# Kernel tuning notes

Hardware: AMD Instinct MI355X
Metric: run time of the kernel (lower is better)

The kernel has to match this reference:

```python
import jax, jax.numpy as jnp
import numpy as np
from jax import lax

D = 256      # d_model
NH = 4       # nhead == len(multi_size)
DH = D // NH # per-head dim = 64
B, H, W = 8, 32, 32
EPS_LN = 1e-5
EPS_ATT = 1e-6


def conv2d(x, w, pad):
    # x: [B,C,H,W], w: [O,I,k,k], SAME padding via pad=k//2
    return lax.conv_general_dilated(
        x, w, window_strides=(1, 1), padding=[(pad, pad), (pad, pad)],
        dimension_numbers=("NCHW", "OIHW", "NCHW"))


def layer_norm(x, g, b):
    m = jnp.mean(x, axis=-1, keepdims=True)
    v = jnp.mean((x - m) ** 2, axis=-1, keepdims=True)
    return (x - m) * lax.rsqrt(v + EPS_LN) * g + b


def setup_inputs() -> dict:
    key = jax.random.key(0)
    ks = jax.random.split(key, 20)
    s = 0.02
    inp = {
        "x": jax.random.normal(ks[0], (B, D, H, W), jnp.float32),
        "source": jax.random.normal(ks[1], (B, D, H, W), jnp.float32),
        # q projection: conv3x3 d_model -> d_model (bias-free)
        "Wq": jax.random.normal(ks[2], (D, D, 3, 3), jnp.float32) * s,
        # MultiConv k projection: kernels 1,3,5,7, each d_model -> dim
        "Wk1": jax.random.normal(ks[3], (DH, D, 1, 1), jnp.float32) * s,
        "Wk3": jax.random.normal(ks[4], (DH, D, 3, 3), jnp.float32) * s,
        "Wk5": jax.random.normal(ks[5], (DH, D, 5, 5), jnp.float32) * s,
        "Wk7": jax.random.normal(ks[6], (DH, D, 7, 7), jnp.float32) * s,
        # MultiConv v projection
        "Wv1": jax.random.normal(ks[7], (DH, D, 1, 1), jnp.float32) * s,
        "Wv3": jax.random.normal(ks[8], (DH, D, 3, 3), jnp.float32) * s,
        "Wv5": jax.random.normal(ks[9], (DH, D, 5, 5), jnp.float32) * s,
        "Wv7": jax.random.normal(ks[10], (DH, D, 7, 7), jnp.float32) * s,
        # merge linear (bias=False), stored [in,out]
        "Wm": jax.random.normal(ks[11], (D, D), jnp.float32) * s,
        "ln1_g": jnp.ones((D,), jnp.float32),
        "ln1_b": jnp.zeros((D,), jnp.float32),
        "ln2_g": jnp.ones((D,), jnp.float32),
        "ln2_b": jnp.zeros((D,), jnp.float32),
        # FF mlp: Linear(2D->2D, no bias), ReLU, Linear(2D->D, no bias); [in,out]
        "W1": jax.random.normal(ks[12], (2 * D, 2 * D), jnp.float32) * s,
        "W2": jax.random.normal(ks[13], (2 * D, D), jnp.float32) * s,
    }
    return inp


def _forward(x, source, Wq, Wk1, Wk3, Wk5, Wk7, Wv1, Wv3, Wv5, Wv7,
             Wm, ln1_g, ln1_b, ln2_g, ln2_b, W1, W2):
    b, c, h, w = x.shape
    h1, w1 = source.shape[2], source.shape[3]
    L = h * w
    S = h1 * w1

    # projections (multi-scale convs -> heads along channel)
    q = conv2d(x, Wq, 1)                                        # [b,D,h,w]
    k = jnp.concatenate([conv2d(source, Wk1, 0), conv2d(source, Wk3, 1),
                         conv2d(source, Wk5, 2), conv2d(source, Wk7, 3)], axis=1)
    v = jnp.concatenate([conv2d(source, Wv1, 0), conv2d(source, Wv3, 1),
                         conv2d(source, Wv5, 2), conv2d(source, Wv7, 3)], axis=1)

    # b c h w -> b (h w) (nhead dim) -> b L nhead dim
    q = q.transpose(0, 2, 3, 1).reshape(b, L, NH, DH)
    k = k.transpose(0, 2, 3, 1).reshape(b, S, NH, DH)
    v = v.transpose(0, 2, 3, 1).reshape(b, S, NH, DH)

    # FullAttention_vis: softmax attention map [b, L, S, nhead]
    temp = DH ** -0.5
    qk = jnp.einsum("blhd,bshd->blsh", q, k)
    attn_vis = jax.nn.softmax(qk * temp, axis=2)

    # LinearAttention (elu+1 kernel feature map)
    Qf = jax.nn.elu(q) + 1.0
    Kf = jax.nn.elu(k) + 1.0
    v_len = jnp.float32(S)
    vals = v / v_len
    KV = jnp.einsum("bshd,bshv->bhdv", Kf, vals)                # [b,NH,DH,DH]
    Z = 1.0 / (jnp.einsum("blhd,bhd->blh", Qf, Kf.sum(axis=1)) + EPS_ATT)
    msg = jnp.einsum("blhd,bhdv,blh->blhv", Qf, KV, Z) * v_len  # [b,L,NH,DH]

    # merge + norm1
    msg = layer_norm(msg.reshape(b, L, D) @ Wm, ln1_g, ln1_b)

    # FF (mlp): cat -> Linear -> ReLU -> Linear -> norm2
    xf = x.transpose(0, 2, 3, 1).reshape(b, L, c)
    ff = jax.nn.relu(jnp.concatenate([xf, msg], axis=2) @ W1) @ W2
    msg = layer_norm(ff, ln2_g, ln2_b)                          # [b,L,D]
    msg = msg.reshape(b, h, w, c).transpose(0, 3, 1, 2)         # b c h w

    out = x + msg
    # b (h0 w0) (h1 w1) c -> b c h0 w0 h1 w1
    vis = attn_vis.reshape(b, h, w, h1, w1, NH).transpose(0, 5, 1, 2, 3, 4)
    return out, vis


def reference(x, source, Wq, Wk1, Wk3, Wk5, Wk7, Wv1, Wv3, Wv5, Wv7,
              Wm, ln1_g, ln1_b, ln2_g, ln2_b, W1, W2):
    return _forward(x, source, Wq, Wk1, Wk3, Wk5, Wk7, Wv1, Wv3, Wv5, Wv7,
                    Wm, ln1_g, ln1_b, ln2_g, ln2_b, W1, W2)
```

## Files before the change

### kernel.cpp

```cpp
#include <hip/hip_runtime.h>

#define DEV __device__ __forceinline__

typedef unsigned short u16;
typedef unsigned int u32;
typedef __bf16 bf16x8 __attribute__((ext_vector_type(8)));
typedef float f32x4 __attribute__((ext_vector_type(4)));

DEV float elu1(float x) { return x > 0.f ? x + 1.f : __expf(x); }

DEV u16 f2bf(float f) {
    union { float f; unsigned u; } v; v.f = f;
    unsigned r = v.u + 0x7fffu + ((v.u >> 16) & 1u);
    return (u16)(r >> 16);
}

DEV float bf2f(u16 h) {
    union { u32 u; float f; } v; v.u = ((u32)h) << 16; return v.f;
}

__global__ __launch_bounds__(256) void prep1_kernel(
    const float* __restrict__ Wq,
    const float* __restrict__ Wk1, const float* __restrict__ Wk3,
    const float* __restrict__ Wk5, const float* __restrict__ Wk7,
    const float* __restrict__ Wv1, const float* __restrict__ Wv3,
    const float* __restrict__ Wv5, const float* __restrict__ Wv7,
    u16* __restrict__ wpack,
    const float* __restrict__ x, const float* __restrict__ src,
    u16* __restrict__ xbh, u16* __restrict__ sbh)
{
    __shared__ float lds[32 * 129];
    const int t = threadIdx.x;
    if (blockIdx.x < 1632) {
        int gid = blockIdx.x * 256 + t;
        int frag = gid >> 6, l = gid & 63;
        const float* W; int K, ocbase = 0, rel;
        if (frag < 1152) {
            W = Wq; K = 3; int slot = frag / 288; rel = frag % 288; ocbase = slot * 64;
        } else {
            int f = frag - 1152; int side = f / 2688; f %= 2688;
            if (f < 32)        { W = side ? Wv1 : Wk1; K = 1; rel = f; }
            else if (f < 320)  { W = side ? Wv3 : Wk3; K = 3; rel = f - 32; }
            else if (f < 1120) { W = side ? Wv5 : Wk5; K = 5; rel = f - 320; }
            else               { W = side ? Wv7 : Wk7; K = 7; rel = f - 1120; }
        }
        int og = rel & 3, cc = (rel >> 2) & 7, tap = rel >> 5;
        int dy = tap / K, dx = tap % K;
        int oc = ocbase + og * 16 + (l & 15);
        int c0 = cc * 32 + (l >> 4) * 8;
        u16 pk[8];
#pragma unroll
        for (int j = 0; j < 8; ++j)
            pk[j] = f2bf(W[((size_t)(oc * 256 + c0 + j) * K + dy) * K + dx]);
        *(int4*)&wpack[(size_t)frag * 512 + l * 8] = *(const int4*)pk;
        return;
    }
    const int i = blockIdx.x - 1632;
    const int inp = i >> 9, rem = i & 511;
    const int b = rem >> 6, cc = (rem >> 3) & 7, pxb = rem & 7;
    const float* in = (inp ? src : x) + ((size_t)b * 256 + cc * 32) * 1024 + pxb * 128;
    u16* outp = (inp ? sbh : xbh) + (size_t)b * 262144 + (size_t)cc * 32768 + pxb * 128 * 32;
#pragma unroll
    for (int u = 0; u < 4; ++u) {
        int unit = t + u * 256;
        int r = unit >> 5, px4 = unit & 31;
        float4 v = *(const float4*)(in + (size_t)r * 1024 + px4 * 4);
        lds[r * 129 + px4 * 4 + 0] = v.x;
        lds[r * 129 + px4 * 4 + 1] = v.y;
        lds[r * 129 + px4 * 4 + 2] = v.z;
        lds[r * 129 + px4 * 4 + 3] = v.w;
    }
    __syncthreads();
#pragma unroll
    for (int u = 0; u < 2; ++u) {
        int unit = t + u * 256;
        int px = unit >> 2, cg = unit & 3;
        u16 pk[8];
#pragma unroll
        for (int j = 0; j < 8; ++j) pk[j] = f2bf(lds[(cg * 8 + j) * 129 + px]);
        *(int4*)&outp[px * 32 + cg * 8] = *(const int4*)pk;
    }
}

template<int K>
DEV void conv_mfma_body(const u16* __restrict__ srcb,
                        const u16* __restrict__ wsec,
                        float* __restrict__ dst,
                        u16* Bt, int y0, int cch0, int ncc, int t)
{
    constexpr int P = K / 2;
    const int w = t >> 6, l = t & 63;
    const int chi = l >> 4, ln = l & 15;
    const int rowbase = chi * 22 + w * 2 + 3 - P;
    const int colbase = ln + 3 - P;
    f32x4 acc[4][4];
#pragma unroll
    for (int m = 0; m < 4; ++m)
#pragma unroll
        for (int n = 0; n < 4; ++n) acc[m][n] = (f32x4){0.f, 0.f, 0.f, 0.f};

    for (int cc = 0; cc < ncc; ++cc) {
        const int ccg = cch0 + cc;
        __syncthreads();
#pragma unroll
        for (int u = 0; u < 7; ++u) {
            int unit = t + (u << 9);
            if (unit < 2816) {
                int xv = unit & 31, r = unit >> 5;
                int yy = r % 22, ch = r / 22;
                int ygl = y0 - 3 + yy;
                int4 pk;
                if ((unsigned)ygl < 32u)
                    pk = *(const int4*)&srcb[(size_t)ccg * 32768 + (ygl * 32 + xv) * 32 + ch * 8];
                else
                    pk = (int4){0, 0, 0, 0};
                *(int4*)&Bt[((ch * 22 + yy) * 40 + xv + 3) * 8] = pk;
            } else if (unit < 3520) {
                int hu = unit - 2816;
                int hx = hu & 7; int xi = hx < 3 ? hx : hx + 32;
                int r = hu >> 3; int yy = r % 22, ch = r / 22;
                int4 z = {0, 0, 0, 0};
                *(int4*)&Bt[((ch * 22 + yy) * 40 + xi) * 8] = z;
            }
        }
        __syncthreads();
#pragma unroll
        for (int dy = 0; dy < K; ++dy) {
#pragma unroll
            for (int dx = 0; dx < K; ++dx) {
                const int tap = dy * K + dx;
                const u16* wp = wsec + ((size_t)(tap * 8 + ccg) * 4) * 512 + l * 8;
                bf16x8 a0 = *(const bf16x8*)(wp);
                bf16x8 a1 = *(const bf16x8*)(wp + 512);
                bf16x8 a2 = *(const bf16x8*)(wp + 1024);
                bf16x8 a3 = *(const bf16x8*)(wp + 1536);
                bf16x8 bf[4];
#pragma unroll
                for (int n = 0; n < 4; ++n) {
                    int row = rowbase + dy + (n >> 1);
                    int col = colbase + dx + (n & 1) * 16;
                    bf[n] = *(const bf16x8*)&Bt[(row * 40 + col) * 8];
                }
#pragma unroll
                for (int n = 0; n < 4; ++n) {
                    acc[0][n] = __builtin_amdgcn_mfma_f32_16x16x32_bf16(a0, bf[n], acc[0][n], 0, 0, 0);
                    acc[1][n] = __builtin_amdgcn_mfma_f32_16x16x32_bf16(a1, bf[n], acc[1][n], 0, 0, 0);
                    acc[2][n] = __builtin_amdgcn_mfma_f32_16x16x32_bf16(a2, bf[n], acc[2][n], 0, 0, 0);
                    acc[3][n] = __builtin_amdgcn_mfma_f32_16x16x32_bf16(a3, bf[n], acc[3][n], 0, 0, 0);
                }
            }
        }
    }
#pragma unroll
    for (int m = 0; m < 4; ++m)
#pragma unroll
        for (int n = 0; n < 4; ++n) {
            int y = y0 + w * 2 + (n >> 1);
            int px = y * 32 + (n & 1) * 16 + ln;
            int ocb = m * 16 + chi * 4;
#pragma unroll
            for (int r = 0; r < 4; ++r)
                dst[(size_t)(ocb + r) * 1024 + px] = acc[m][n][r];
        }
}

__global__ __launch_bounds__(512) void conv_mfma_kernel(
    const u16* __restrict__ xbh, const u16* __restrict__ sbh,
    const u16* __restrict__ wpack,
    float* __restrict__ qb, float* __restrict__ kb, float* __restrict__ vb,
    float* __restrict__ p5, float* __restrict__ p7)
{
    __shared__ u16 Bt[4 * 22 * 40 * 8];
    const int bx = blockIdx.x, t = threadIdx.x;
    const int g = bx & 31, b = (bx >> 5) & 7, m = bx >> 8;
    if (g < 4) {
        conv_mfma_body<3>(xbh + (size_t)b * 262144,
                          wpack + (size_t)(g * 288) * 512,
                          qb + ((size_t)b * 256 + g * 64) * 1024,
                          Bt, m * 16, 0, 8, t);
        return;
    }
    const int gs = g - 4;
    const int side = gs / 14, gg = gs % 14;
    const u16* sp = sbh + (size_t)b * 262144;
    float* fin = side ? vb : kb;
    const size_t wkb = 1152 + (size_t)side * 2688;
    if (gg == 0) {
        conv_mfma_body<1>(sp, wpack + (wkb + 0) * 512,
                          fin + ((size_t)b * 256) * 1024, Bt, m * 16, 0, 8, t);
    } else if (gg == 1) {
        conv_mfma_body<3>(sp, wpack + (wkb + 32) * 512,
                          fin + ((size_t)b * 256 + 64) * 1024, Bt, m * 16, 0, 8, t);
    } else if (gg < 6) {
        int cpart = gg - 2;
        conv_mfma_body<5>(sp, wpack + (wkb + 320) * 512,
                          p5 + (((size_t)side * 4 + cpart) * 8 + b) * 65536,
                          Bt, m * 16, cpart * 2, 2, t);
    } else {
        int cpart = gg - 6;
        conv_mfma_body<7>(sp, wpack + (wkb + 1120) * 512,
                          p7 + (((size_t)side * 8 + cpart) * 8 + b) * 65536,
                          Bt, m * 16, cpart, 1, t);
    }
}

__global__ __launch_bounds__(256) void prep2_kernel(
    const float* __restrict__ p5, const float* __restrict__ p7,
    float* __restrict__ kb, float* __restrict__ vb,
    const float* __restrict__ W1, const float* __restrict__ W2,
    const float* __restrict__ Wm,
    u16* __restrict__ w1p, u16* __restrict__ w2p, u16* __restrict__ wmp)
{
    const int t = threadIdx.x;
    if (blockIdx.x < 2048) {
        int gid = blockIdx.x * 256 + t;
        int px4 = gid & 255;
        int rr = gid >> 8;
        int oc = rr & 63, b = (rr >> 6) & 7, head = (rr >> 9) & 1, side = rr >> 10;
        float* outb = side ? vb : kb;
        float4 s = make_float4(0.f, 0.f, 0.f, 0.f);
        if (head == 0) {
#pragma unroll
            for (int p = 0; p < 4; ++p) {
                float4 u = *((const float4*)(p5 + (((size_t)side * 4 + p) * 8 + b) * 65536 + (size_t)oc * 1024) + px4);
                s.x += u.x; s.y += u.y; s.z += u.z; s.w += u.w;
            }
            *((float4*)(outb + ((size_t)b * 256 + 128 + oc) * 1024) + px4) = s;
        } else {
#pragma unroll
            for (int p = 0; p < 8; ++p) {
                float4 u = *((const float4*)(p7 + (((size_t)side * 8 + p) * 8 + b) * 65536 + (size_t)oc * 1024) + px4);
                s.x += u.x; s.y += u.y; s.z += u.z; s.w += u.w;
            }
            *((float4*)(outb + ((size_t)b * 256 + 192 + oc) * 1024) + px4) = s;
        }
        return;
    }
    int gid = (blockIdx.x - 2048) * 256 + t;
    int f = gid >> 6, l = gid & 63;
    if (f >= 896) return;
    u16 pk[8];
    if (f < 512) {
        int ks = f >> 5, nf = f & 31;
#pragma unroll
        for (int j = 0; j < 8; ++j)
            pk[j] = f2bf(W1[(size_t)(ks * 32 + (l >> 4) * 8 + j) * 512 + nf * 16 + (l & 15)]);
        *(int4*)&w1p[(size_t)f * 512 + l * 8] = *(const int4*)pk;
    } else if (f < 768) {
        int f2 = f - 512;
        int ks = f2 >> 4, nf = f2 & 15;
#pragma unroll
        for (int j = 0; j < 8; ++j)
            pk[j] = f2bf(W2[(size_t)(ks * 32 + (l >> 4) * 8 + j) * 256 + nf * 16 + (l & 15)]);
        *(int4*)&w2p[(size_t)f2 * 512 + l * 8] = *(const int4*)pk;
    } else {
        int f3 = f - 768;
        int ks = f3 >> 4, nf = f3 & 15;
#pragma unroll
        for (int j = 0; j < 8; ++j)
            pk[j] = f2bf(Wm[(size_t)(ks * 32 + (l >> 4) * 8 + j) * 256 + nf * 16 + (l & 15)]);
        *(int4*)&wmp[(size_t)f3 * 512 + l * 8] = *(const int4*)pk;
    }
}

__global__ __launch_bounds__(256) void prep3_kernel(
    const float* __restrict__ qb, const float* __restrict__ kb,
    const float* __restrict__ vb,
    u16* __restrict__ qbt, u16* __restrict__ kbt,
    float* __restrict__ KVp, float* __restrict__ Ksump)
{
    __shared__ float4 smem4[2112];
    const int t = threadIdx.x;
    if (blockIdx.x < 1024) {
        float* lds = (float*)smem4;
        const int i = blockIdx.x;
        const int inp = i >> 9, rem = i & 511;
        const int b = rem >> 6, h = (rem >> 4) & 3, pxb = rem & 15;
        const float* in = (inp ? kb : qb) + ((size_t)b * 256 + h * 64) * 1024 + pxb * 64;
        u16* outp = (inp ? kbt : qbt) + (((size_t)(b * 4 + h)) * 1024 + pxb * 64) * 64;
#pragma unroll
        for (int u = 0; u < 4; ++u) {
            int unit = t + u * 256;
            int r = unit >> 4, px4 = unit & 15;
            float4 v = *(const float4*)(in + (size_t)r * 1024 + px4 * 4);
            lds[r * 65 + px4 * 4 + 0] = v.x;
            lds[r * 65 + px4 * 4 + 1] = v.y;
            lds[r * 65 + px4 * 4 + 2] = v.z;
            lds[r * 65 + px4 * 4 + 3] = v.w;
        }
        __syncthreads();
#pragma unroll
        for (int u = 0; u < 2; ++u) {
            int unit = t + u * 256;
            int px = unit >> 3, cg = unit & 7;
            u16 pk[8];
#pragma unroll
            for (int j = 0; j < 8; ++j) pk[j] = f2bf(lds[(cg * 8 + j) * 65 + px]);
            *(int4*)&outp[px * 64 + cg * 8] = *(const int4*)pk;
        }
        return;
    }
    float4* Kt4 = smem4;
    float4* Vt4 = smem4 + 64 * 17;
    float* Kt = (float*)Kt4;
    float* Vt = (float*)Vt4;
    const int bx = blockIdx.x - 1024;
    const int b = bx >> 4, h = (bx >> 2) & 3, ch = bx & 3;
    const float* kp = kb + ((size_t)b * 256 + h * 64) * 1024 + ch * 256;
    const float* vp = vb + ((size_t)b * 256 + h * 64) * 1024 + ch * 256;
    const int d = t >> 2, v0 = (t & 3) * 16;
    float4 acc[4];
#pragma unroll
    for (int j = 0; j < 4; ++j) acc[j] = make_float4(0.f, 0.f, 0.f, 0.f);
    float ks = 0.f;
    for (int st = 0; st < 4; ++st) {
        __syncthreads();
        {
            int dd = t >> 2, r0 = (t & 3) * 16;
#pragma unroll
            for (int mm = 0; mm < 4; ++mm) {
                float4 kv = *(const float4*)(kp + dd * 1024 + st * 64 + r0 + mm * 4);
                Kt[(r0 + mm * 4 + 0) * 68 + dd] = elu1(kv.x);
                Kt[(r0 + mm * 4 + 1) * 68 + dd] = elu1(kv.y);
                Kt[(r0 + mm * 4 + 2) * 68 + dd] = elu1(kv.z);
                Kt[(r0 + mm * 4 + 3) * 68 + dd] = elu1(kv.w);
                float4 vv = *(const float4*)(vp + dd * 1024 + st * 64 + r0 + mm * 4);
                Vt[(r0 + mm * 4 + 0) * 64 + dd] = vv.x;
                Vt[(r0 + mm * 4 + 1) * 64 + dd] = vv.y;
                Vt[(r0 + mm * 4 + 2) * 64 + dd] = vv.z;
                Vt[(r0 + mm * 4 + 3) * 64 + dd] = vv.w;
            }
        }
        __syncthreads();
#pragma unroll 8
        for (int s = 0; s < 64; ++s) {
            float kf = Kt[s * 68 + d];
            const float4* vvp = (const float4*)(Vt + s * 64 + v0);
#pragma unroll
            for (int j = 0; j < 4; ++j) {
                float4 vv = vvp[j];
                acc[j].x += kf * vv.x; acc[j].y += kf * vv.y;
                acc[j].z += kf * vv.z; acc[j].w += kf * vv.w;
            }
        }
        if (t < 64) {
#pragma unroll 8
            for (int s = 0; s < 64; ++s) ks += Kt[s * 68 + t];
        }
    }
    float* op = KVp + ((size_t)((ch * 32 + b * 4 + h) * 64 + d)) * 64 + v0;
#pragma unroll
    for (int j = 0; j < 4; ++j) ((float4*)op)[j] = acc[j];
    if (t < 64) Ksump[(size_t)(ch * 32 + b * 4 + h) * 64 + t] = ks;
}

__global__ __launch_bounds__(512) void qk_sm_msg_kernel(
    const u16* __restrict__ qbt, const u16* __restrict__ kbt,
    float* __restrict__ vis,
    const float* __restrict__ KVp, const float* __restrict__ Ksump,
    float* __restrict__ msg)
{
    __shared__ float4 smem4[4178];
    const int t = threadIdx.x;
    if (blockIdx.x < 1024) {
        u16* kf = (u16*)smem4;
        u16* qf = (u16*)smem4 + 32 * 512;
        float* redM = (float*)((char*)smem4 + 36864);
        float* redS = redM + 256;
        const int bx = blockIdx.x;
        const int b = bx >> 7, h = (bx >> 5) & 3, l0 = (bx & 31) * 32;
        const u16* qtp = qbt + ((size_t)(b * 4 + h)) * 1024 * 64;
        const u16* ktp = kbt + ((size_t)(b * 4 + h)) * 1024 * 64;

        if (t < 256) {
            int r = t & 31, dblk = t >> 5;
            int4 pk = *(const int4*)&qtp[(size_t)(l0 + r) * 64 + dblk * 8];
            *(int4*)&qf[(((r >> 4) * 2 + (dblk >> 2)) * 64 + (dblk & 3) * 16 + (r & 15)) * 8] = pk;
        }
        __syncthreads();

        const int w = t >> 6, l = t & 63, ln = l & 15, lg = l >> 4;
        bf16x8 a[2][2];
#pragma unroll
        for (int fr = 0; fr < 2; ++fr)
#pragma unroll
            for (int ks = 0; ks < 2; ++ks)
                a[fr][ks] = *(const bf16x8*)&qf[((fr * 2 + ks) * 64 + l) * 8];

        f32x4 acc[2][4][2];
#pragma unroll
        for (int fr = 0; fr < 2; ++fr)
#pragma unroll
            for (int cc = 0; cc < 4; ++cc)
#pragma unroll
                for (int f = 0; f < 2; ++f) acc[fr][cc][f] = (f32x4){0.f, 0.f, 0.f, 0.f};

#pragma unroll
        for (int cc = 0; cc < 4; ++cc) {
            __syncthreads();
#pragma unroll
            for (int it = 0; it < 4; ++it) {
                int unit = it * 512 + t;
                int sl = unit & 255, dblk = unit >> 8;
                int4 pk = *(const int4*)&ktp[(size_t)(cc * 256 + sl) * 64 + dblk * 8];
                *(int4*)&kf[(((sl >> 4) * 2 + (dblk >> 2)) * 64 + (dblk & 3) * 16 + (sl & 15)) * 8] = pk;
            }
            __syncthreads();
#pragma unroll
            for (int f = 0; f < 2; ++f) {
                int fg = (w * 2 + f) * 2;
                bf16x8 b0 = *(const bf16x8*)&kf[((fg + 0) * 64 + l) * 8];
                bf16x8 b1 = *(const bf16x8*)&kf[((fg + 1) * 64 + l) * 8];
#pragma unroll
                for (int fr = 0; fr < 2; ++fr) {
                    acc[fr][cc][f] = __builtin_amdgcn_mfma_f32_16x16x32_bf16(a[fr][0], b0, acc[fr][cc][f], 0, 0, 0);
                    acc[fr][cc][f] = __builtin_amdgcn_mfma_f32_16x16x32_bf16(a[fr][1], b1, acc[fr][cc][f], 0, 0, 0);
                }
            }
        }

#pragma unroll
        for (int fr = 0; fr < 2; ++fr)
#pragma unroll
            for (int cc = 0; cc < 4; ++cc)
#pragma unroll
                for (int f = 0; f < 2; ++f)
#pragma unroll
                    for (int e = 0; e < 4; ++e) acc[fr][cc][f][e] *= 0.125f;

        float rmax[2][4];
#pragma unroll
        for (int fr = 0; fr < 2; ++fr)
#pragma unroll
            for (int reg = 0; reg < 4; ++reg) {
                float m = -1e30f;
#pragma unroll
                for (int cc = 0; cc < 4; ++cc)
#pragma unroll
                    for (int f = 0; f < 2; ++f) m = fmaxf(m, acc[fr][cc][f][reg]);
#pragma unroll
                for (int off = 1; off < 16; off <<= 1) m = fmaxf(m, __shfl_xor(m, off));
                if (ln == 0) redM[(fr * 16 + lg * 4 + reg) * 8 + w] = m;
                rmax[fr][reg] = m;
            }
        __syncthreads();
#pragma unroll
        for (int fr = 0; fr < 2; ++fr)
#pragma unroll
            for (int reg = 0; reg < 4; ++reg) {
                int r = fr * 16 + lg * 4 + reg;
                float m = redM[r * 8];
#pragma unroll
                for (int ww = 1; ww < 8; ++ww) m = fmaxf(m, redM[r * 8 + ww]);
                rmax[fr][reg] = m;
            }
#pragma unroll
        for (int fr = 0; fr < 2; ++fr)
#pragma unroll
            for (int reg = 0; reg < 4; ++reg) {
                float s = 0.f;
                float m = rmax[fr][reg];
#pragma unroll
                for (int cc = 0; cc < 4; ++cc)
#pragma unroll
                    for (int f = 0; f < 2; ++f) {
                        float e = __expf(acc[fr][cc][f][reg] - m);
                        acc[fr][cc][f][reg] = e;
                        s += e;
                    }
#pragma unroll
                for (int off = 1; off < 16; off <<= 1) s += __shfl_xor(s, off);
                if (ln == 0) redS[(fr * 16 + lg * 4 + reg) * 8 + w] = s;
            }
        __syncthreads();
        float invv[2][4];
#pragma unroll
        for (int fr = 0; fr < 2; ++fr)
#pragma unroll
            for (int reg = 0; reg < 4; ++reg) {
                int r = fr * 16 + lg * 4 + reg;
                float s = redS[r * 8] + redS[r * 8 + 1] + redS[r * 8 + 2] + redS[r * 8 + 3]
                        + redS[r * 8 + 4] + redS[r * 8 + 5] + redS[r * 8 + 6] + redS[r * 8 + 7];
                invv[fr][reg] = 1.f / s;
            }
        float* outT = (float*)smem4;
        float* visp = vis + (((size_t)(b * 4 + h)) << 20);
#pragma unroll
        for (int cc = 0; cc < 4; ++cc) {
            __syncthreads();
#pragma unroll
            for (int fr = 0; fr < 2; ++fr)
#pragma unroll
                for (int reg = 0; reg < 4; ++reg) {
                    int r = fr * 16 + lg * 4 + reg;
#pragma unroll
                    for (int f = 0; f < 2; ++f)
                        outT[r * 260 + w * 32 + f * 16 + ln] = acc[fr][cc][f][reg] * invv[fr][reg];
                }
            __syncthreads();
#pragma unroll
            for (int u = 0; u < 4; ++u) {
                int unit = u * 512 + t;
                int r = unit >> 6, c4 = unit & 63;
                float4 v = *(const float4*)&outT[r * 260 + c4 * 4];
                *(float4*)&visp[(size_t)(l0 + r) * 1024 + cc * 256 + c4 * 4] = v;
            }
        }
        return;
    }
    float* kvl = (float*)smem4;
    float* ksl = (float*)smem4 + 4 * 4112;
    const int bx2 = blockIdx.x - 1024;
    const int b = bx2 >> 3, l0 = (bx2 & 7) * 128;
#pragma unroll
    for (int m = 0; m < 8; ++m) {
        int unit = t + (m << 9);
        int hh = unit >> 10, dd = (unit >> 4) & 63, v4 = unit & 15;
        float4 s = make_float4(0.f, 0.f, 0.f, 0.f);
#pragma unroll
        for (int ch = 0; ch < 4; ++ch) {
            float4 u = *(const float4*)&KVp[((size_t)(ch * 32 + b * 4)) * 4096 + (size_t)unit * 4];
            s.x += u.x; s.y += u.y; s.z += u.z; s.w += u.w;
        }
        *(float4*)&kvl[hh * 4112 + dd * 64 + v4 * 4] = s;
    }
    if (t < 256) {
        float s = 0.f;
#pragma unroll
        for (int ch = 0; ch < 4; ++ch)
            s += Ksump[(size_t)(ch * 32 + b * 4) * 64 + t];
        ksl[(t >> 6) * 65 + (t & 63)] = s;
    }
    __syncthreads();
    const int h = t & 3, l = l0 + (t >> 2);
    const u16* qrow = qbt + ((size_t)(b * 4 + h) * 1024 + l) * 64;
    float qf[64];
#pragma unroll
    for (int j8 = 0; j8 < 8; ++j8) {
        int4 pk = *(const int4*)&qrow[j8 * 8];
        const u16* pku = (const u16*)&pk;
#pragma unroll
        for (int e = 0; e < 8; ++e) qf[j8 * 8 + e] = elu1(bf2f(pku[e]));
    }
    float zd = 1e-6f;
#pragma unroll
    for (int dd = 0; dd < 64; ++dd) zd += qf[dd] * ksl[h * 65 + dd];
    const float Z = 1.f / zd;
    float* op = msg + ((size_t)(b * 1024 + l)) * 256 + h * 64;
    for (int c0 = 0; c0 < 64; c0 += 16) {
        float4 a[4];
#pragma unroll
        for (int j = 0; j < 4; ++j) a[j] = make_float4(0.f, 0.f, 0.f, 0.f);
#pragma unroll
        for (int dd = 0; dd < 64; ++dd) {
            float qv = qf[dd];
            const float4* kp = (const float4*)(kvl + h * 4112 + dd * 64 + c0);
#pragma unroll
            for (int j = 0; j < 4; ++j) {
                float4 kk = kp[j];
                a[j].x += qv * kk.x; a[j].y += qv * kk.y;
                a[j].z += qv * kk.z; a[j].w += qv * kk.w;
            }
        }
#pragma unroll
        for (int j = 0; j < 4; ++j) {
            a[j].x *= Z; a[j].y *= Z; a[j].z *= Z; a[j].w *= Z;
            ((float4*)(op + c0))[j] = a[j];
        }
    }
}

__global__ __launch_bounds__(256) void ff_fused_kernel(
    const float* __restrict__ x, const float* __restrict__ msg,
    const u16* __restrict__ wmp,
    const u16* __restrict__ w1p, const u16* __restrict__ w2p,
    const float* __restrict__ g1, const float* __restrict__ b1,
    const float* __restrict__ g2, const float* __restrict__ b2,
    float* __restrict__ out)
{
    __shared__ u16 tile[16 * 520];
    __shared__ u16 mtile[16 * 264];
    __shared__ float redS[16 * 4];
    __shared__ float redQ[16 * 4];
    float* tf = (float*)tile;
    const int t = threadIdx.x;
    const int base = blockIdx.x * 16;
    const int b = base >> 10, l0 = base & 1023;
    const int w = t >> 6, l = t & 63, ln = l & 15, lg = l >> 4;

    {
        int rr = t & 15, cg = t >> 4;
        for (int cci = 0; cci < 16; ++cci) {
            int c = cci * 16 + cg;
            tile[rr * 520 + c] = f2bf(x[((size_t)b * 256 + c) * 1024 + l0 + rr]);
        }
        int r = t >> 4, cb = (t & 15) * 16;
#pragma unroll
        for (int i = 0; i < 4; ++i) {
            float4 v = *(const float4*)&msg[((size_t)(base + r)) * 256 + cb + i * 4];
            u32 p0 = (u32)f2bf(v.x) | ((u32)f2bf(v.y) << 16);
            u32 p1 = (u32)f2bf(v.z) | ((u32)f2bf(v.w) << 16);
            *(u32*)&mtile[r * 264 + cb + i * 4] = p0;
            *(u32*)&mtile[r * 264 + cb + i * 4 + 2] = p1;
        }
    }
    __syncthreads();

    f32x4 accm[4];
#pragma unroll
    for (int fc = 0; fc < 4; ++fc) accm[fc] = (f32x4){0.f, 0.f, 0.f, 0.f};
    for (int ks = 0; ks < 8; ++ks) {
        bf16x8 a0 = *(const bf16x8*)&mtile[ln * 264 + ks * 32 + lg * 8];
#pragma unroll
        for (int fc = 0; fc < 4; ++fc) {
            bf16x8 bb = *(const bf16x8*)&wmp[((size_t)(ks * 16 + w * 4 + fc) * 64 + l) * 8];
            accm[fc] = __builtin_amdgcn_mfma_f32_16x16x32_bf16(a0, bb, accm[fc], 0, 0, 0);
        }
    }
#pragma unroll
    for (int reg = 0; reg < 4; ++reg) {
        float s = 0.f, qsum = 0.f;
#pragma unroll
        for (int fc = 0; fc < 4; ++fc) {
            float v = accm[fc][reg];
            s += v; qsum += v * v;
        }
#pragma unroll
        for (int off = 1; off < 16; off <<= 1) {
            s += __shfl_xor(s, off);
            qsum += __shfl_xor(qsum, off);
        }
        if (ln == 0) {
            int r = lg * 4 + reg;
            redS[r * 4 + w] = s;
            redQ[r * 4 + w] = qsum;
        }
    }
    __syncthreads();
#pragma unroll
    for (int fc = 0; fc < 4; ++fc) {
        int c = w * 64 + fc * 16 + ln;
        float gg = g1[c], bb = b1[c];
#pragma unroll
        for (int reg = 0; reg < 4; ++reg) {
            int r = lg * 4 + reg;
            float s = redS[r * 4] + redS[r * 4 + 1] + redS[r * 4 + 2] + redS[r * 4 + 3];
            float qs = redQ[r * 4] + redQ[r * 4 + 1] + redQ[r * 4 + 2] + redQ[r * 4 + 3];
            float mean = s * (1.f / 256.f);
            float rstd = rsqrtf(qs * (1.f / 256.f) - mean * mean + 1e-5f);
            tile[r * 520 + 256 + c] = f2bf((accm[fc][reg] - mean) * rstd * gg + bb);
        }
    }
    __syncthreads();

    f32x4 acc1[8];
#pragma unroll
    for (int fc = 0; fc < 8; ++fc) acc1[fc] = (f32x4){0.f, 0.f, 0.f, 0.f};
    for (int ks = 0; ks < 16; ++ks) {
        bf16x8 a0 = *(const bf16x8*)&tile[ln * 520 + ks * 32 + lg * 8];
#pragma unroll
        for (int fc = 0; fc < 8; ++fc) {
            bf16x8 bb = *(const bf16x8*)&w1p[((size_t)(ks * 32 + w * 8 + fc) * 64 + l) * 8];
            acc1[fc] = __builtin_amdgcn_mfma_f32_16x16x32_bf16(a0, bb, acc1[fc], 0, 0, 0);
        }
    }
    __syncthreads();
#pragma unroll
    for (int fc = 0; fc < 8; ++fc)
#pragma unroll
        for (int reg = 0; reg < 4; ++reg) {
            int r = lg * 4 + reg;
            int c = w * 128 + fc * 16 + ln;
            tile[r * 520 + c] = f2bf(fmaxf(acc1[fc][reg], 0.f));
        }
    __syncthreads();

    f32x4 acc2[4];
#pragma unroll
    for (int fc = 0; fc < 4; ++fc) acc2[fc] = (f32x4){0.f, 0.f, 0.f, 0.f};
    for (int ks = 0; ks < 16; ++ks) {
        bf16x8 a0 = *(const bf16x8*)&tile[ln * 520 + ks * 32 + lg * 8];
#pragma unroll
        for (int fc = 0; fc < 4; ++fc) {
            bf16x8 bb = *(const bf16x8*)&w2p[((size_t)(ks * 16 + w * 4 + fc) * 64 + l) * 8];
            acc2[fc] = __builtin_amdgcn_mfma_f32_16x16x32_bf16(a0, bb, acc2[fc], 0, 0, 0);
        }
    }
#pragma unroll
    for (int reg = 0; reg < 4; ++reg) {
        float s = 0.f, qsum = 0.f;
#pragma unroll
        for (int fc = 0; fc < 4; ++fc) {
            float v = acc2[fc][reg];
            s += v; qsum += v * v;
        }
#pragma unroll
        for (int off = 1; off < 16; off <<= 1) {
            s += __shfl_xor(s, off);
            qsum += __shfl_xor(qsum, off);
        }
        if (ln == 0) {
            int r = lg * 4 + reg;
            redS[r * 4 + w] = s;
            redQ[r * 4 + w] = qsum;
        }
    }
    __syncthreads();
    float mean[4], rstd[4];
#pragma unroll
    for (int reg = 0; reg < 4; ++reg) {
        int r = lg * 4 + reg;
        float s = redS[r * 4] + redS[r * 4 + 1] + redS[r * 4 + 2] + redS[r * 4 + 3];
        float qs = redQ[r * 4] + redQ[r * 4 + 1] + redQ[r * 4 + 2] + redQ[r * 4 + 3];
        float m = s * (1.f / 256.f);
        mean[reg] = m;
        rstd[reg] = rsqrtf(qs * (1.f / 256.f) - m * m + 1e-5f);
    }
    __syncthreads();
#pragma unroll
    for (int fc = 0; fc < 4; ++fc) {
        int c = w * 64 + fc * 16 + ln;
        float gg = g2[c], bb = b2[c];
#pragma unroll
        for (int reg = 0; reg < 4; ++reg) {
            int r = lg * 4 + reg;
            tf[r * 260 + c] = (acc2[fc][reg] - mean[reg]) * rstd[reg] * gg + bb;
        }
    }
    __syncthreads();
    {
        const float* xp = x + ((size_t)b * 256 + t) * 1024 + l0;
        float* op = out + ((size_t)b * 256 + t) * 1024 + l0;
#pragma unroll
        for (int i = 0; i < 4; ++i) {
            float4 xv = *(const float4*)(xp + i * 4);
            float4 o;
            o.x = xv.x + tf[(i * 4 + 0) * 260 + t];
            o.y = xv.y + tf[(i * 4 + 1) * 260 + t];
            o.z = xv.z + tf[(i * 4 + 2) * 260 + t];
            o.w = xv.w + tf[(i * 4 + 3) * 260 + t];
            *(float4*)(op + i * 4) = o;
        }
    }
}

extern "C" void kernel_launch(void* const* d_in, const int* in_sizes, int n_in,
                              void* d_out, int out_size, void* d_ws, size_t ws_size,
                              hipStream_t stream)
{
    const float* x    = (const float*)d_in[0];
    const float* src  = (const float*)d_in[1];
    const float* Wq   = (const float*)d_in[2];
    const float* Wk1  = (const float*)d_in[3];
    const float* Wk3  = (const float*)d_in[4];
    const float* Wk5  = (const float*)d_in[5];
    const float* Wk7  = (const float*)d_in[6];
    const float* Wv1  = (const float*)d_in[7];
    const float* Wv3  = (const float*)d_in[8];
    const float* Wv5  = (const float*)d_in[9];
    const float* Wv7  = (const float*)d_in[10];
    const float* Wm   = (const float*)d_in[11];
    const float* g1   = (const float*)d_in[12];
    const float* b1   = (const float*)d_in[13];
    const float* g2   = (const float*)d_in[14];
    const float* b2   = (const float*)d_in[15];
    const float* W1   = (const float*)d_in[16];
    const float* W2   = (const float*)d_in[17];

    float* out = (float*)d_out;
    float* vis = out + 2097152;

    float* p5 = vis;
    float* p7 = vis + 4194304;

    float* ws    = (float*)d_ws;
    float* qb    = ws;
    float* kb    = ws + 2097152;
    float* vb    = ws + 4194304;
    u16*   wpack = (u16*)(ws + 6291456);
    u16*   w1p   = (u16*)(ws + 6291456);
    u16*   w2p   = (u16*)(ws + 6422528);
    u16*   wmp   = (u16*)(ws + 6488064);
    u16*   qbt   = (u16*)(ws + 6520832);
    u16*   kbt   = (u16*)(ws + 7569408);
    u16*   xbh   = (u16*)(ws + 7962624);
    u16*   sbh   = (u16*)(ws + 9011200);
    float* msg   = ws + 10059776;
    float* KVp   = ws + 12156928;
    float* Ksump = ws + 12681216;

    prep1_kernel    <<<2656, 256, 0, stream>>>(Wq, Wk1, Wk3, Wk5, Wk7,
                                               Wv1, Wv3, Wv5, Wv7, wpack,
                                               x, src, xbh, sbh);
    conv_mfma_kernel<<<512,  512, 0, stream>>>(xbh, sbh, wpack, qb, kb, vb, p5, p7);
    prep2_kernel    <<<2272, 256, 0, stream>>>(p5, p7, kb, vb,
                                               W1, W2, Wm, w1p, w2p, wmp);
    prep3_kernel    <<<1152, 256, 0, stream>>>(qb, kb, vb, qbt, kbt, KVp, Ksump);
    qk_sm_msg_kernel<<<1088, 512, 0, stream>>>(qbt, kbt, vis, KVp, Ksump, msg);
    ff_fused_kernel <<<512,  256, 0, stream>>>(x, msg, wmp, w1p, w2p,
                                               g1, b1, g2, b2, out);
}
```

Before: 269.1 us.

## Emit conv outputs as pixel-major bf16 and drop the separate transpose pass

The conv MFMA kernel now packs its accumulators to bf16 and writes them in pixel-major [px][64] layout, so the Q/K/V projections and the 5x5/7x7 partial sums no longer go through fp32 channel-major buffers. The split-K reduction in prep2 reads bf16 partials, and the transpose/convert half of prep3 is removed, which cuts several hundred blocks and a large amount of memory traffic. The attention-map store to vis now uses nontemporal stores. In exchange, partial sums are rounded to bf16 before they are reduced, which adds some error, and K/V reach the KV computation already rounded.

```diff
diff --git a/kernel.cpp b/kernel.cpp
--- a/kernel.cpp
+++ b/kernel.cpp
@@ -85,7 +85,7 @@
 template<int K>
 DEV void conv_mfma_body(const u16* __restrict__ srcb,
                         const u16* __restrict__ wsec,
-                        float* __restrict__ dst,
+                        u16* __restrict__ dst,
                         u16* Bt, int y0, int cch0, int ncc, int t)
 {
     constexpr int P = K / 2;
@@ -158,17 +158,18 @@
             int y = y0 + w * 2 + (n >> 1);
             int px = y * 32 + (n & 1) * 16 + ln;
             int ocb = m * 16 + chi * 4;
-#pragma unroll
-            for (int r = 0; r < 4; ++r)
-                dst[(size_t)(ocb + r) * 1024 + px] = acc[m][n][r];
+            u16 pk[4];
+#pragma unroll
+            for (int r = 0; r < 4; ++r) pk[r] = f2bf(acc[m][n][r]);
+            *(uint2*)&dst[(size_t)px * 64 + ocb] = *(const uint2*)pk;
         }
 }
 
 __global__ __launch_bounds__(512) void conv_mfma_kernel(
     const u16* __restrict__ xbh, const u16* __restrict__ sbh,
     const u16* __restrict__ wpack,
-    float* __restrict__ qb, float* __restrict__ kb, float* __restrict__ vb,
-    float* __restrict__ p5, float* __restrict__ p7)
+    u16* __restrict__ qbt, u16* __restrict__ kbt, u16* __restrict__ vbt,
+    u16* __restrict__ p5u, u16* __restrict__ p7u)
 {
     __shared__ u16 Bt[4 * 22 * 40 * 8];
     const int bx = blockIdx.x, t = threadIdx.x;
@@ -176,67 +177,76 @@
     if (g < 4) {
         conv_mfma_body<3>(xbh + (size_t)b * 262144,
                           wpack + (size_t)(g * 288) * 512,
-                          qb + ((size_t)b * 256 + g * 64) * 1024,
+                          qbt + ((size_t)(b * 4 + g)) * 65536,
                           Bt, m * 16, 0, 8, t);
         return;
     }
     const int gs = g - 4;
     const int side = gs / 14, gg = gs % 14;
     const u16* sp = sbh + (size_t)b * 262144;
-    float* fin = side ? vb : kb;
+    u16* fin = side ? vbt : kbt;
     const size_t wkb = 1152 + (size_t)side * 2688;
     if (gg == 0) {
         conv_mfma_body<1>(sp, wpack + (wkb + 0) * 512,
-                          fin + ((size_t)b * 256) * 1024, Bt, m * 16, 0, 8, t);
+                          fin + ((size_t)(b * 4 + 0)) * 65536, Bt, m * 16, 0, 8, t);
     } else if (gg == 1) {
         conv_mfma_body<3>(sp, wpack + (wkb + 32) * 512,
-                          fin + ((size_t)b * 256 + 64) * 1024, Bt, m * 16, 0, 8, t);
+                          fin + ((size_t)(b * 4 + 1)) * 65536, Bt, m * 16, 0, 8, t);
     } else if (gg < 6) {
         int cpart = gg - 2;
         conv_mfma_body<5>(sp, wpack + (wkb + 320) * 512,
-                          p5 + (((size_t)side * 4 + cpart) * 8 + b) * 65536,
+                          p5u + (((size_t)side * 4 + cpart) * 8 + b) * 65536,
                           Bt, m * 16, cpart * 2, 2, t);
     } else {
         int cpart = gg - 6;
         conv_mfma_body<7>(sp, wpack + (wkb + 1120) * 512,
-                          p7 + (((size_t)side * 8 + cpart) * 8 + b) * 65536,
+                          p7u + (((size_t)side * 8 + cpart) * 8 + b) * 65536,
                           Bt, m * 16, cpart, 1, t);
     }
 }
 
 __global__ __launch_bounds__(256) void prep2_kernel(
-    const float* __restrict__ p5, const float* __restrict__ p7,
-    float* __restrict__ kb, float* __restrict__ vb,
+    const u16* __restrict__ p5u, const u16* __restrict__ p7u,
+    u16* __restrict__ kbt, u16* __restrict__ vbt,
     const float* __restrict__ W1, const float* __restrict__ W2,
     const float* __restrict__ Wm,
     u16* __restrict__ w1p, u16* __restrict__ w2p, u16* __restrict__ wmp)
 {
     const int t = threadIdx.x;
-    if (blockIdx.x < 2048) {
+    if (blockIdx.x < 1024) {
         int gid = blockIdx.x * 256 + t;
-        int px4 = gid & 255;
-        int rr = gid >> 8;
-        int oc = rr & 63, b = (rr >> 6) & 7, head = (rr >> 9) & 1, side = rr >> 10;
-        float* outb = side ? vb : kb;
-        float4 s = make_float4(0.f, 0.f, 0.f, 0.f);
-        if (head == 0) {
+        int u8 = gid & 8191;
+        int b = (gid >> 13) & 7;
+        int headk = (gid >> 16) & 1;
+        int side = gid >> 17;
+        float sacc[8];
+#pragma unroll
+        for (int e = 0; e < 8; ++e) sacc[e] = 0.f;
+        if (headk == 0) {
 #pragma unroll
             for (int p = 0; p < 4; ++p) {
-                float4 u = *((const float4*)(p5 + (((size_t)side * 4 + p) * 8 + b) * 65536 + (size_t)oc * 1024) + px4);
-                s.x += u.x; s.y += u.y; s.z += u.z; s.w += u.w;
-            }
-            *((float4*)(outb + ((size_t)b * 256 + 128 + oc) * 1024) + px4) = s;
+                int4 u = *(const int4*)&p5u[(((size_t)side * 4 + p) * 8 + b) * 65536 + (size_t)u8 * 8];
+                const u16* uu = (const u16*)&u;
+#pragma unroll
+                for (int e = 0; e < 8; ++e) sacc[e] += bf2f(uu[e]);
+            }
         } else {
 #pragma unroll
             for (int p = 0; p < 8; ++p) {
-                float4 u = *((const float4*)(p7 + (((size_t)side * 8 + p) * 8 + b) * 65536 + (size_t)oc * 1024) + px4);
-                s.x += u.x; s.y += u.y; s.z += u.z; s.w += u.w;
-            }
-            *((float4*)(outb + ((size_t)b * 256 + 192 + oc) * 1024) + px4) = s;
-        }
+                int4 u = *(const int4*)&p7u[(((size_t)side * 8 + p) * 8 + b) * 65536 + (size_t)u8 * 8];
+                const u16* uu = (const u16*)&u;
+#pragma unroll
+                for (int e = 0; e < 8; ++e) sacc[e] += bf2f(uu[e]);
+            }
+        }
+        u16 pk[8];
+#pragma unroll
+        for (int e = 0; e < 8; ++e) pk[e] = f2bf(sacc[e]);
+        u16* outb = side ? vbt : kbt;
+        *(int4*)&outb[((size_t)(b * 4 + 2 + headk)) * 65536 + (size_t)u8 * 8] = *(const int4*)pk;
         return;
     }
-    int gid = (blockIdx.x - 2048) * 256 + t;
+    int gid = (blockIdx.x - 1024) * 256 + t;
     int f = gid >> 6, l = gid & 63;
     if (f >= 896) return;
     u16 pk[8];
@@ -264,50 +274,17 @@
 }
 
 __global__ __launch_bounds__(256) void prep3_kernel(
-    const float* __restrict__ qb, const float* __restrict__ kb,
-    const float* __restrict__ vb,
-    u16* __restrict__ qbt, u16* __restrict__ kbt,
+    const u16* __restrict__ kbt, const u16* __restrict__ vbt,
     float* __restrict__ KVp, float* __restrict__ Ksump)
 {
     __shared__ float4 smem4[2112];
+    float* Kt = (float*)smem4;
+    float* Vt = (float*)(smem4 + 64 * 17);
     const int t = threadIdx.x;
-    if (blockIdx.x < 1024) {
-        float* lds = (float*)smem4;
-        const int i = blockIdx.x;
-        const int inp = i >> 9, rem = i & 511;
-        const int b = rem >> 6, h = (rem >> 4) & 3, pxb = rem & 15;
-        const float* in = (inp ? kb : qb) + ((size_t)b * 256 + h * 64) * 1024 + pxb * 64;
-        u16* outp = (inp ? kbt : qbt) + (((size_t)(b * 4 + h)) * 1024 + pxb * 64) * 64;
-#pragma unroll
-        for (int u = 0; u < 4; ++u) {
-            int unit = t + u * 256;
-            int r = unit >> 4, px4 = unit & 15;
-            float4 v = *(const float4*)(in + (size_t)r * 1024 + px4 * 4);
-            lds[r * 65 + px4 * 4 + 0] = v.x;
-            lds[r * 65 + px4 * 4 + 1] = v.y;
-            lds[r * 65 + px4 * 4 + 2] = v.z;
-            lds[r * 65 + px4 * 4 + 3] = v.w;
-        }
-        __syncthreads();
-#pragma unroll
-        for (int u = 0; u < 2; ++u) {
-            int unit = t + u * 256;
-            int px = unit >> 3, cg = unit & 7;
-            u16 pk[8];
-#pragma unroll
-            for (int j = 0; j < 8; ++j) pk[j] = f2bf(lds[(cg * 8 + j) * 65 + px]);
-            *(int4*)&outp[px * 64 + cg * 8] = *(const int4*)pk;
-        }
-        return;
-    }
-    float4* Kt4 = smem4;
-    float4* Vt4 = smem4 + 64 * 17;
-    float* Kt = (float*)Kt4;
-    float* Vt = (float*)Vt4;
-    const int bx = blockIdx.x - 1024;
+    const int bx = blockIdx.x;
     const int b = bx >> 4, h = (bx >> 2) & 3, ch = bx & 3;
-    const float* kp = kb + ((size_t)b * 256 + h * 64) * 1024 + ch * 256;
-    const float* vp = vb + ((size_t)b * 256 + h * 64) * 1024 + ch * 256;
+    const u16* kbase = kbt + ((size_t)(b * 4 + h) * 1024 + ch * 256) * 64;
+    const u16* vbase = vbt + ((size_t)(b * 4 + h) * 1024 + ch * 256) * 64;
     const int d = t >> 2, v0 = (t & 3) * 16;
     float4 acc[4];
 #pragma unroll
@@ -316,19 +293,20 @@
     for (int st = 0; st < 4; ++st) {
         __syncthreads();
         {
-            int dd = t >> 2, r0 = (t & 3) * 16;
-#pragma unroll
-            for (int mm = 0; mm < 4; ++mm) {
-                float4 kv = *(const float4*)(kp + dd * 1024 + st * 64 + r0 + mm * 4);
-                Kt[(r0 + mm * 4 + 0) * 68 + dd] = elu1(kv.x);
-                Kt[(r0 + mm * 4 + 1) * 68 + dd] = elu1(kv.y);
-                Kt[(r0 + mm * 4 + 2) * 68 + dd] = elu1(kv.z);
-                Kt[(r0 + mm * 4 + 3) * 68 + dd] = elu1(kv.w);
-                float4 vv = *(const float4*)(vp + dd * 1024 + st * 64 + r0 + mm * 4);
-                Vt[(r0 + mm * 4 + 0) * 64 + dd] = vv.x;
-                Vt[(r0 + mm * 4 + 1) * 64 + dd] = vv.y;
-                Vt[(r0 + mm * 4 + 2) * 64 + dd] = vv.z;
-                Vt[(r0 + mm * 4 + 3) * 64 + dd] = vv.w;
+            int s = t >> 2, d0 = (t & 3) * 16;
+            const u16* krow = kbase + (size_t)(st * 64 + s) * 64;
+            const u16* vrow = vbase + (size_t)(st * 64 + s) * 64;
+#pragma unroll
+            for (int oo = 0; oo < 2; ++oo) {
+                int4 k8 = *(const int4*)&krow[d0 + oo * 8];
+                int4 v8 = *(const int4*)&vrow[d0 + oo * 8];
+                const u16* ku = (const u16*)&k8;
+                const u16* vu = (const u16*)&v8;
+#pragma unroll
+                for (int e = 0; e < 8; ++e) {
+                    Kt[s * 68 + d0 + oo * 8 + e] = elu1(bf2f(ku[e]));
+                    Vt[s * 64 + d0 + oo * 8 + e] = bf2f(vu[e]);
+                }
             }
         }
         __syncthreads();
@@ -502,8 +480,9 @@
             for (int u = 0; u < 4; ++u) {
                 int unit = u * 512 + t;
                 int r = unit >> 6, c4 = unit & 63;
-                float4 v = *(const float4*)&outT[r * 260 + c4 * 4];
-                *(float4*)&visp[(size_t)(l0 + r) * 1024 + cc * 256 + c4 * 4] = v;
+                f32x4 v = *(const f32x4*)&outT[r * 260 + c4 * 4];
+                __builtin_nontemporal_store(v,
+                    (f32x4*)&visp[(size_t)(l0 + r) * 1024 + cc * 256 + c4 * 4]);
             }
         }
         return;
@@ -770,19 +749,17 @@
     float* out = (float*)d_out;
     float* vis = out + 2097152;
 
-    float* p5 = vis;
-    float* p7 = vis + 4194304;
+    u16* p5u = (u16*)vis;
+    u16* p7u = (u16*)(vis + 2097152);
 
     float* ws    = (float*)d_ws;
-    float* qb    = ws;
-    float* kb    = ws + 2097152;
-    float* vb    = ws + 4194304;
+    u16*   qbt   = (u16*)ws;
+    u16*   kbt   = (u16*)(ws + 1048576);
+    u16*   vbt   = (u16*)(ws + 2097152);
     u16*   wpack = (u16*)(ws + 6291456);
     u16*   w1p   = (u16*)(ws + 6291456);
     u16*   w2p   = (u16*)(ws + 6422528);
     u16*   wmp   = (u16*)(ws + 6488064);
-    u16*   qbt   = (u16*)(ws + 6520832);
-    u16*   kbt   = (u16*)(ws + 7569408);
     u16*   xbh   = (u16*)(ws + 7962624);
     u16*   sbh   = (u16*)(ws + 9011200);
     float* msg   = ws + 10059776;
@@ -792,10 +769,11 @@
     prep1_kernel    <<<2656, 256, 0, stream>>>(Wq, Wk1, Wk3, Wk5, Wk7,
                                                Wv1, Wv3, Wv5, Wv7, wpack,
                                                x, src, xbh, sbh);
-    conv_mfma_kernel<<<512,  512, 0, stream>>>(xbh, sbh, wpack, qb, kb, vb, p5, p7);
-    prep2_kernel    <<<2272, 256, 0, stream>>>(p5, p7, kb, vb,
+    conv_mfma_kernel<<<512,  512, 0, stream>>>(xbh, sbh, wpack, qbt, kbt, vbt,
+                                               p5u, p7u);
+    prep2_kernel    <<<1248, 256, 0, stream>>>(p5u, p7u, kbt, vbt,
                                                W1, W2, Wm, w1p, w2p, wmp);
-    prep3_kernel    <<<1152, 256, 0, stream>>>(qb, kb, vb, qbt, kbt, KVp, Ksump);
+    prep3_kernel    <<<128,  256, 0, stream>>>(kbt, vbt, KVp, Ksump);
     qk_sm_msg_kernel<<<1088, 512, 0, stream>>>(qbt, kbt, vis, KVp, Ksump, msg);
     ff_fused_kernel <<<512,  256, 0, stream>>>(x, msg, wmp, w1p, w2p,
                                                g1, b1, g2, b2, out);
```

New measurement: 260.7 us. 1.03x faster.
